# Performance work log

Hardware: AMD Instinct MI355X
Metric: run time of the kernel (lower is better)

Reference implementation:

```python
import jax, jax.numpy as jnp
import numpy as np

B, L, C = 2, 2048, 1024
DK, H = 64, 16

def setup_inputs() -> dict:
    key = jax.random.key(0)
    ks = jax.random.split(key, 12)
    def lin(kw, kb, out_dim, in_dim):
        w = jax.random.normal(kw, (out_dim, in_dim), jnp.float32) * (1.0 / np.sqrt(in_dim))
        b = jnp.zeros((out_dim,), jnp.float32)
        return w, b
    WQ_w, WQ_b = lin(ks[0], ks[1], DK * H, C)
    WK_w, WK_b = lin(ks[2], ks[3], DK * H, C)
    WV_w, WV_b = lin(ks[4], ks[5], DK * H, C)
    WO_w, WO_b = lin(ks[6], ks[7], C, DK * H)
    qx = jax.random.normal(ks[8], (B, L, C), jnp.float32)
    kx = jax.random.normal(ks[9], (B, L, C), jnp.float32)
    vx = jax.random.normal(ks[10], (B, L, C), jnp.float32)
    maskPAD = jax.random.randint(ks[11], (B, L, L), 0, 2, jnp.int32)
    return {"qx": qx, "kx": kx, "vx": vx, "maskPAD": maskPAD,
            "WQ_w": WQ_w, "WQ_b": WQ_b, "WK_w": WK_w, "WK_b": WK_b,
            "WV_w": WV_w, "WV_b": WV_b, "WO_w": WO_w, "WO_b": WO_b}

def reference(qx, kx, vx, maskPAD, WQ_w, WQ_b, WK_w, WK_b, WV_w, WV_b, WO_w, WO_b):
    Bq, qL, _ = qx.shape
    kvL = kx.shape[1]
    # projections -> [B, H, L, DK]
    q = (qx @ WQ_w.T + WQ_b).reshape(Bq, qL, H, DK).transpose(0, 2, 1, 3)
    k = (kx @ WK_w.T + WK_b).reshape(Bq, kvL, H, DK).transpose(0, 2, 1, 3)
    v = (vx @ WV_w.T + WV_b).reshape(Bq, kvL, H, DK).transpose(0, 2, 1, 3)
    scores = jnp.einsum('bhqd,bhkd->bhqk', q, k) / np.sqrt(DK).astype(np.float32)
    scores = jnp.where((maskPAD == 0)[:, None, :, :], jnp.float32(-2**15 + 1), scores)
    alpha = jax.nn.softmax(scores, axis=3)  # dropout p=0 (eval)
    z = jnp.einsum('bhqk,bhkd->bhqd', alpha, v)
    z = z.transpose(0, 2, 1, 3).reshape(Bq, qL, H * DK)
    return z @ WO_w.T + WO_b
```

## Files before the change

### kernel.cpp

```cpp
#include <hip/hip_runtime.h>
#include <stdint.h>
#include <math.h>

typedef short short8 __attribute__((ext_vector_type(8)));
typedef short short4v __attribute__((ext_vector_type(4)));
typedef float float4v __attribute__((ext_vector_type(4)));

static __device__ __forceinline__ float bf2f(uint16_t u) {
    union { uint32_t i; float f; } x; x.i = ((uint32_t)u) << 16; return x.f;
}
static __device__ __forceinline__ uint16_t f2bf(float f) {
    union { float f; uint32_t i; } x; x.f = f;
    uint32_t u = x.i;
    u += 0x7FFFu + ((u >> 16) & 1u);
    return (uint16_t)(u >> 16);
}
static __device__ __forceinline__ uint16_t f2bf_sane(float f) {
    uint16_t u = f2bf(f);
    if ((u & 0x7F80u) == 0x7F80u) u = 0;
    return u;
}
static __device__ __forceinline__ float san_f32(float f) {
    union { float f; uint32_t i; } x; x.f = f;
    if (((x.i >> 23) & 0xFFu) == 0xFFu) return 0.f;
    return x.f;
}
static __device__ __forceinline__ void gll16(const void* g, void* l) {
    __builtin_amdgcn_global_load_lds((const __attribute__((address_space(1))) void*)g,
                                     (__attribute__((address_space(3))) void*)l,
                                     16, 0, 0);
}
static __device__ __forceinline__ short8 load8(const void* p, size_t off, int fp32) {
    if (!fp32) return *(const short8*)((const uint16_t*)p + off);
    const float* f = (const float*)p + off;
    const float4v a = *(const float4v*)f;
    const float4v b = *(const float4v*)(f + 4);
    short8 r;
    r[0] = (short)f2bf(a[0]); r[1] = (short)f2bf(a[1]);
    r[2] = (short)f2bf(a[2]); r[3] = (short)f2bf(a[3]);
    r[4] = (short)f2bf(b[0]); r[5] = (short)f2bf(b[1]);
    r[6] = (short)f2bf(b[2]); r[7] = (short)f2bf(b[3]);
    return r;
}

static __device__ __forceinline__ float4v mfma16_bf16(short4v a, short4v b, float4v c) {
#if __has_builtin(__builtin_amdgcn_mfma_f32_16x16x16bf16_1k)
    return __builtin_amdgcn_mfma_f32_16x16x16bf16_1k(a, b, c, 0, 0, 0);
#else
    float4v d = c;
    asm volatile("v_mfma_f32_16x16x16_bf16 %0, %1, %2, %0"
                 : "+v"(d) : "v"(a), "v"(b));
    return d;
#endif
}

__global__ __launch_bounds__(256) void detect_kernel(const uint16_t* qx, int* flag)
{
    __shared__ int s;
    const int tid = threadIdx.x;
    if (tid == 0) s = 0;
    __syncthreads();
    int bad = 0;
#pragma unroll 8
    for (int i = 0; i < 64; ++i) {
        const uint16_t u = qx[tid * 64 + i];
        bad |= ((u & 0x7F80u) == 0x7F80u) ? 1 : 0;
    }
    if (bad) atomicOr(&s, 1);
    __syncthreads();
    if (tid == 0) *flag = s;
}

__global__ __launch_bounds__(256) void pack_kernel(
    const int* __restrict__ mask, uint64_t* __restrict__ mask64)
{
    const int wave = threadIdx.x >> 6, lane = threadIdx.x & 63;
    const int row = blockIdx.x * 4 + wave;
    const int* src = mask + (size_t)row * 2048;
#pragma unroll 4
    for (int j = 0; j < 32; ++j) {
        const int m = src[j * 64 + lane];
        const uint64_t bal = __ballot(m != 0);
        if (lane == 0) mask64[(size_t)row * 32 + j] = bal;
    }
}

__global__ __launch_bounds__(256) void convert_kernel(
    const void* qx, const void* kx, const void* vx,
    const void* wq, const void* wk, const void* wv, const void* wo,
    const void* bq, const void* bk, const void* bv, const void* bo,
    uint16_t* cIn, uint16_t* cW, uint16_t* cB, const int* flag)
{
    const int mode = *flag;
    if (!mode) return;
    const int z = blockIdx.z;
    if (z < 3) {
        const void* src = (z == 0) ? qx : (z == 1) ? kx : vx;
        uint16_t* dst = cIn + (size_t)z * 4194304;
#pragma unroll
        for (int it = 0; it < 8; ++it) {
            const int idx8 = (blockIdx.x * 8 + it) * 256 + threadIdx.x;
            *(short8*)(dst + (size_t)idx8 * 8) = load8(src, (size_t)idx8 * 8, 1);
        }
    } else if (z < 7) {
        const int t = z - 3;
        const void* src = (t == 0) ? wq : (t == 1) ? wk : (t == 2) ? wv : wo;
        uint16_t* dst = cW + (size_t)t * 1048576;
#pragma unroll
        for (int it = 0; it < 2; ++it) {
            const int idx8 = (blockIdx.x * 2 + it) * 256 + threadIdx.x;
            *(short8*)(dst + (size_t)idx8 * 8) = load8(src, (size_t)idx8 * 8, 1);
        }
    } else {
        const int idx8 = blockIdx.x * 256 + threadIdx.x;
        if (idx8 < 128) {
#pragma unroll
            for (int t = 0; t < 4; ++t) {
                const void* src = (t == 0) ? bq : (t == 1) ? bk : (t == 2) ? bv : bo;
                *(short8*)(cB + t * 1024 + idx8 * 8) = load8(src, (size_t)idx8 * 8, 1);
            }
        }
    }
}

template <int MI, int NI>
static __device__ __forceinline__ void gemm_tile(
    const uint16_t* __restrict__ A, const uint16_t* __restrict__ W,
    const uint16_t* __restrict__ bias, void* __restrict__ C,
    int c_fp32, float out_scale)
{
    constexpr int TM = MI * 32, TN = NI * 32;
    __shared__ __align__(16) uint16_t sA[TM * 32];
    __shared__ __align__(16) uint16_t sB[TN * 32];

    const int tid  = threadIdx.x;
    const int wave = tid >> 6;
    const int lane = tid & 63;
    const int quad = lane >> 4;
    const int l15  = lane & 15;
    const int m0 = blockIdx.y * TM;
    const int n0 = blockIdx.x * TN;
    const int wm = (wave >> 1) * (MI * 16);
    const int wn = (wave & 1) * (NI * 16);
    const int r16 = lane >> 2;
    const int ch  = lane & 3;

    float4v acc[MI][NI] = {};

    for (int k0 = 0; k0 < 1024; k0 += 32) {
        __syncthreads();
#pragma unroll
        for (int g = wave; g < TM / 16; g += 4)
            gll16(A + (size_t)(m0 + g * 16 + r16) * 1024 + k0 + ch * 8,
                  (char*)sA + (size_t)g * 1024);
#pragma unroll
        for (int g = wave; g < TN / 16; g += 4)
            gll16(W + (size_t)(n0 + g * 16 + r16) * 1024 + k0 + ch * 8,
                  (char*)sB + (size_t)g * 1024);
        asm volatile("s_waitcnt vmcnt(0)" ::: "memory");
        __syncthreads();

        short8 af[MI], bfr[NI];
#pragma unroll
        for (int i = 0; i < MI; ++i)
            af[i] = *(const short8*)&sA[(wm + i * 16 + l15) * 32 + quad * 8];
#pragma unroll
        for (int j = 0; j < NI; ++j)
            bfr[j] = *(const short8*)&sB[(wn + j * 16 + l15) * 32 + quad * 8];
#pragma unroll
        for (int mi = 0; mi < MI; ++mi)
#pragma unroll
            for (int ni = 0; ni < NI; ++ni)
                acc[mi][ni] = __builtin_amdgcn_mfma_f32_16x16x32_bf16(
                    af[mi], bfr[ni], acc[mi][ni], 0, 0, 0);
    }

#pragma unroll
    for (int ni = 0; ni < NI; ++ni) {
        const int n = n0 + wn + ni * 16 + l15;
        const float bv = bf2f(bias[n]);
#pragma unroll
        for (int mi = 0; mi < MI; ++mi) {
            const int mbase = m0 + wm + mi * 16 + quad * 4;
#pragma unroll
            for (int r = 0; r < 4; ++r) {
                const float v = (acc[mi][ni][r] + bv) * out_scale;
                const size_t idx = (size_t)(mbase + r) * 1024 + n;
                if (c_fp32) ((float*)C)[idx] = san_f32(v);
                else        ((uint16_t*)C)[idx] = f2bf_sane(v);
            }
        }
    }
}

__global__ __launch_bounds__(256) void qkv_kernel(
    const uint16_t* rqx, const uint16_t* rkx, const uint16_t* rvx,
    const uint16_t* rwq, const uint16_t* rwk, const uint16_t* rwv,
    const uint16_t* rbq, const uint16_t* rbk, const uint16_t* rbv,
    const uint16_t* cIn, const uint16_t* cW, const uint16_t* cB,
    uint16_t* Q, uint16_t* K, uint16_t* V, const int* flag)
{
    const int mode = *flag;
    const int z = blockIdx.z;
    const uint16_t* A = mode ? cIn + (size_t)z * 4194304
                             : ((z == 0) ? rqx : (z == 1) ? rkx : rvx);
    const uint16_t* W = mode ? cW + (size_t)z * 1048576
                             : ((z == 0) ? rwq : (z == 1) ? rwk : rwv);
    const uint16_t* b = mode ? cB + z * 1024
                             : ((z == 0) ? rbq : (z == 1) ? rbk : rbv);
    uint16_t* C = (z == 0) ? Q : (z == 1) ? K : V;
    const float sc = (z == 0) ? 0.125f : 1.0f;
    gemm_tile<4, 4>(A, W, b, C, 0, sc);
}

__global__ __launch_bounds__(256) void out_kernel(
    const uint16_t* Z, const uint16_t* rwo, const uint16_t* rbo,
    const uint16_t* cW, const uint16_t* cB, void* out, const int* flag)
{
    const int mode = *flag;
    const uint16_t* W = mode ? cW + 3 * 1048576 : rwo;
    const uint16_t* b = mode ? cB + 3 * 1024 : rbo;
    gemm_tile<2, 4>(Z, W, b, out, mode, 1.0f);
}

__global__ __launch_bounds__(256) void vtrans_kernel(
    const uint16_t* __restrict__ Vp, uint16_t* __restrict__ Vt)
{
    __shared__ __align__(16) uint16_t t[64][72];
    const int tid = threadIdx.x;
    const int lt = blockIdx.x, h = blockIdx.y, b = blockIdx.z;
#pragma unroll
    for (int p = 0; p < 2; ++p) {
        const int r = p * 32 + (tid >> 3);
        const int c = (tid & 7) * 8;
        *(short8*)&t[r][c] =
            *(const short8*)(Vp + (size_t)(b * 2048 + lt * 64 + r) * 1024 + h * 64 + c);
    }
    __syncthreads();
#pragma unroll
    for (int p = 0; p < 2; ++p) {
        const int d = p * 32 + (tid >> 3);
        const int c = (tid & 7) * 8;
        short8 v;
#pragma unroll
        for (int j = 0; j < 8; ++j) v[j] = (short)t[c + j][d];
        *(short8*)(Vt + (size_t)((b * 16 + h) * 64 + d) * 2048 + lt * 64 + c) = v;
    }
}

#define VS 72

__global__ __launch_bounds__(256, 4) void attn_kernel(
    const uint16_t* __restrict__ Q, const uint16_t* __restrict__ Kp,
    const uint16_t* __restrict__ Vt, const uint64_t* __restrict__ mask64,
    uint16_t* __restrict__ Oa, uint16_t* __restrict__ Ob,
    float* __restrict__ lpart)
{
    __shared__ __align__(16) uint16_t sK[64 * VS];
    __shared__ __align__(16) uint16_t sV[64 * VS];

    const int tid = threadIdx.x;
    const int wave = tid >> 6, lane = tid & 63;
    const int quad = lane >> 4, l15 = lane & 15;
    const int qt = blockIdx.x, h = blockIdx.y;
    const int b = blockIdx.z & 1, half = blockIdx.z >> 1;
    const int q0 = qt * 128;
    const int qw = q0 + wave * 32;

    const int srow = tid >> 2;
    const int sc0  = tid & 3;

    short8 qf[2][2];
#pragma unroll
    for (int mi = 0; mi < 2; ++mi)
#pragma unroll
        for (int kk = 0; kk < 2; ++kk)
            qf[mi][kk] = *(const short8*)(Q + (size_t)(b * 2048 + qw + mi * 16 + l15) * 1024
                                            + h * 64 + (quad + 4 * kk) * 8);

    const uint64_t* mrow[2];
#pragma unroll
    for (int mj = 0; mj < 2; ++mj)
        mrow[mj] = mask64 + (size_t)(b * 2048 + qw + mj * 16 + l15) * 32;

    float4v oaccT[4][2] = {};
    float lsum[2] = {};

    const int kt_lo = half * 16, kt_hi = kt_lo + 16;
    for (int kt = kt_lo; kt < kt_hi; ++kt) {
        const int k0 = kt * 64;
        const short8 kx0 = *(const short8*)(Kp + (size_t)(b * 2048 + k0 + srow) * 1024 + h * 64 + sc0 * 8);
        const short8 kx1 = *(const short8*)(Kp + (size_t)(b * 2048 + k0 + srow) * 1024 + h * 64 + (sc0 + 4) * 8);
        const short8 vx0 = *(const short8*)(Vt + (size_t)((b * 16 + h) * 64 + srow) * 2048 + k0 + sc0 * 8);
        const short8 vx1 = *(const short8*)(Vt + (size_t)((b * 16 + h) * 64 + srow) * 2048 + k0 + (sc0 + 4) * 8);
        const uint64_t mw0 = mrow[0][kt];
        const uint64_t mw1 = mrow[1][kt];
        __syncthreads();
        *(short8*)&sK[srow * VS + sc0 * 8]       = kx0;
        *(short8*)&sK[srow * VS + (sc0 + 4) * 8] = kx1;
        *(short8*)&sV[srow * VS + sc0 * 8]       = vx0;
        *(short8*)&sV[srow * VS + (sc0 + 4) * 8] = vx1;
        __syncthreads();

        float4v sacc[2][4] = {};
#pragma unroll
        for (int ni = 0; ni < 4; ++ni) {
            const int row = ni * 16 + l15;
#pragma unroll
            for (int kk = 0; kk < 2; ++kk) {
                const short8 kf = *(const short8*)&sK[row * VS + (quad + 4 * kk) * 8];
                sacc[0][ni] = __builtin_amdgcn_mfma_f32_16x16x32_bf16(kf, qf[0][kk], sacc[0][ni], 0, 0, 0);
                sacc[1][ni] = __builtin_amdgcn_mfma_f32_16x16x32_bf16(kf, qf[1][kk], sacc[1][ni], 0, 0, 0);
            }
        }

        short4v pf[2][4];
#pragma unroll
        for (int mj = 0; mj < 2; ++mj) {
            const uint64_t mw = mj ? mw1 : mw0;
#pragma unroll
            for (int ni = 0; ni < 4; ++ni) {
                const uint32_t nib = (uint32_t)(mw >> (ni * 16 + quad * 4)) & 0xFu;
                short4v t;
#pragma unroll
                for (int r = 0; r < 4; ++r) {
                    const float p = (nib >> r) & 1u ? __expf(sacc[mj][ni][r]) : 0.f;
                    lsum[mj] += p;
                    t[r] = (short)f2bf(p);
                }
                pf[mj][ni] = t;
            }
        }

#pragma unroll
        for (int di = 0; di < 4; ++di) {
            const int row = di * 16 + l15;
#pragma unroll
            for (int ni = 0; ni < 4; ++ni) {
                const short4v vf = *(const short4v*)&sV[row * VS + ni * 16 + quad * 4];
                oaccT[di][0] = mfma16_bf16(vf, pf[0][ni], oaccT[di][0]);
                oaccT[di][1] = mfma16_bf16(vf, pf[1][ni], oaccT[di][1]);
            }
        }
    }

#if !__has_builtin(__builtin_amdgcn_mfma_f32_16x16x16bf16_1k)
    asm volatile("s_nop 7\ns_nop 7\ns_nop 7" ::: "memory");
#endif

#pragma unroll
    for (int mj = 0; mj < 2; ++mj) {
        lsum[mj] += __shfl_xor(lsum[mj], 16);
        lsum[mj] += __shfl_xor(lsum[mj], 32);
    }

    uint16_t* Op = half ? Ob : Oa;
#pragma unroll
    for (int mj = 0; mj < 2; ++mj) {
        const int qrow = qw + mj * 16 + l15;
#pragma unroll
        for (int di = 0; di < 4; ++di) {
            short4v o;
#pragma unroll
            for (int r = 0; r < 4; ++r) o[r] = (short)f2bf(oaccT[di][mj][r]);
            *(short4v*)(Op + (size_t)(b * 2048 + qrow) * 1024 + h * 64 + di * 16 + quad * 4) = o;
        }
        if (quad == 0)
            lpart[half * 65536 + (b * 16 + h) * 2048 + qrow] = lsum[mj];
    }
}

__global__ __launch_bounds__(256) void combine_kernel(
    const uint16_t* __restrict__ Oa, const uint16_t* __restrict__ Ob,
    const float* __restrict__ lpart, uint16_t* __restrict__ Z)
{
    const int e8 = blockIdx.x * 256 + threadIdx.x;
    const int flat = e8 * 8;
    const int bh_row = flat >> 10;
    const int h = (flat >> 6) & 15;
    const int b = bh_row >> 11;
    const int row = bh_row & 2047;
    const int lidx = (b * 16 + h) * 2048 + row;
    const float inv = 1.0f / fmaxf(lpart[lidx] + lpart[65536 + lidx], 1e-37f);
    const short8 a = *(const short8*)(Oa + flat);
    const short8 c = *(const short8*)(Ob + flat);
    short8 o;
#pragma unroll
    for (int j = 0; j < 8; ++j)
        o[j] = (short)f2bf_sane((bf2f((uint16_t)a[j]) + bf2f((uint16_t)c[j])) * inv);
    *(short8*)(Z + flat) = o;
}

extern "C" void kernel_launch(void* const* d_in, const int* in_sizes, int n_in,
                              void* d_out, int out_size, void* d_ws, size_t ws_size,
                              hipStream_t stream)
{
    const void* qx  = d_in[0];
    const void* kx  = d_in[1];
    const void* vx  = d_in[2];
    const int*  msk = (const int*)d_in[3];

    char* ws = (char*)d_ws;
    const size_t MB = 1024 * 1024;
    uint16_t* cIn = (uint16_t*)(ws);
    uint16_t* cW  = (uint16_t*)(ws + 24 * MB);
    uint16_t* cB  = (uint16_t*)(ws + 32 * MB);
    int*      flg = (int*)(ws + 32 * MB + 16 * 1024);
    uint16_t* Qb  = (uint16_t*)(ws + 33 * MB);
    uint16_t* Kb  = (uint16_t*)(ws + 41 * MB);
    uint16_t* Vb  = (uint16_t*)(ws + 49 * MB);
    uint64_t* m64 = (uint64_t*)(ws + 57 * MB);
    uint16_t* Vt  = (uint16_t*)(ws + 8 * MB);
    uint16_t* Oa  = (uint16_t*)(ws);
    uint16_t* Ob  = (uint16_t*)(ws + 16 * MB);
    float*    lp  = (float*)(ws + 49 * MB);
    uint16_t* Zb  = Oa;

    detect_kernel<<<1, 256, 0, stream>>>((const uint16_t*)qx, flg);
    pack_kernel<<<1024, 256, 0, stream>>>(msk, m64);
    convert_kernel<<<dim3(256, 1, 8), 256, 0, stream>>>(
        qx, kx, vx, d_in[4], d_in[6], d_in[8], d_in[10],
        d_in[5], d_in[7], d_in[9], d_in[11], cIn, cW, cB, flg);
    qkv_kernel<<<dim3(8, 32, 3), 256, 0, stream>>>(
        (const uint16_t*)qx, (const uint16_t*)kx, (const uint16_t*)vx,
        (const uint16_t*)d_in[4], (const uint16_t*)d_in[6], (const uint16_t*)d_in[8],
        (const uint16_t*)d_in[5], (const uint16_t*)d_in[7], (const uint16_t*)d_in[9],
        cIn, cW, cB, Qb, Kb, Vb, flg);
    vtrans_kernel<<<dim3(32, 16, 2), 256, 0, stream>>>(Vb, Vt);
    attn_kernel<<<dim3(16, 16, 4), 256, 0, stream>>>(Qb, Kb, Vt, m64, Oa, Ob, lp);
    combine_kernel<<<4096, 256, 0, stream>>>(Oa, Ob, lp, Zb);
    out_kernel<<<dim3(8, 64), 256, 0, stream>>>(
        Zb, (const uint16_t*)d_in[10], (const uint16_t*)d_in[11], cW, cB, d_out, flg);
}
```

Baseline: 305.5 us.

## Fuse mask packing into QKV launch and streamline softmax exponent and row sums

```diff
diff --git a/kernel.cpp b/kernel.cpp
--- a/kernel.cpp
+++ b/kernel.cpp
@@ -5,6 +5,7 @@
 typedef short short8 __attribute__((ext_vector_type(8)));
 typedef short short4v __attribute__((ext_vector_type(4)));
 typedef float float4v __attribute__((ext_vector_type(4)));
+typedef unsigned int uint2v __attribute__((ext_vector_type(2)));
 
 static __device__ __forceinline__ float bf2f(uint16_t u) {
     union { uint32_t i; float f; } x; x.i = ((uint32_t)u) << 16; return x.f;
@@ -42,7 +43,17 @@
     r[6] = (short)f2bf(b[2]); r[7] = (short)f2bf(b[3]);
     return r;
 }
-
+static __device__ __forceinline__ float fast_exp2(float x) {
+#if __has_builtin(__builtin_amdgcn_exp2f)
+    return __builtin_amdgcn_exp2f(x);
+#else
+    return exp2f(x);
+#endif
+}
+static __device__ __forceinline__ uint32_t pkbf(float a, float b) {
+    union { float f; uint32_t u; } xa, xb; xa.f = a; xb.f = b;
+    return __builtin_amdgcn_perm(xb.u + 0x8000u, xa.u + 0x8000u, 0x07060302u);
+}
 static __device__ __forceinline__ float4v mfma16_bf16(short4v a, short4v b, float4v c) {
 #if __has_builtin(__builtin_amdgcn_mfma_f32_16x16x16bf16_1k)
     return __builtin_amdgcn_mfma_f32_16x16x16bf16_1k(a, b, c, 0, 0, 0);
@@ -69,20 +80,6 @@
     if (bad) atomicOr(&s, 1);
     __syncthreads();
     if (tid == 0) *flag = s;
-}
-
-__global__ __launch_bounds__(256) void pack_kernel(
-    const int* __restrict__ mask, uint64_t* __restrict__ mask64)
-{
-    const int wave = threadIdx.x >> 6, lane = threadIdx.x & 63;
-    const int row = blockIdx.x * 4 + wave;
-    const int* src = mask + (size_t)row * 2048;
-#pragma unroll 4
-    for (int j = 0; j < 32; ++j) {
-        const int m = src[j * 64 + lane];
-        const uint64_t bal = __ballot(m != 0);
-        if (lane == 0) mask64[(size_t)row * 32 + j] = bal;
-    }
 }
 
 __global__ __launch_bounds__(256) void convert_kernel(
@@ -193,15 +190,33 @@
     }
 }
 
+#define QSCALE 0.180336880f
+
 __global__ __launch_bounds__(256) void qkv_kernel(
     const uint16_t* rqx, const uint16_t* rkx, const uint16_t* rvx,
     const uint16_t* rwq, const uint16_t* rwk, const uint16_t* rwv,
     const uint16_t* rbq, const uint16_t* rbk, const uint16_t* rbv,
     const uint16_t* cIn, const uint16_t* cW, const uint16_t* cB,
-    uint16_t* Q, uint16_t* K, uint16_t* V, const int* flag)
-{
+    uint16_t* Q, uint16_t* K, uint16_t* V, const int* flag,
+    const int* __restrict__ mask, uint64_t* __restrict__ mask64)
+{
+    const int z = blockIdx.z;
+    if (z == 3) {
+        const int wave = threadIdx.x >> 6, lane = threadIdx.x & 63;
+        const int bid = blockIdx.y * 8 + blockIdx.x;
+#pragma unroll
+        for (int rr = 0; rr < 4; ++rr) {
+            const int row = bid * 16 + wave * 4 + rr;
+            const int* src = mask + (size_t)row * 2048;
+#pragma unroll 4
+            for (int j = 0; j < 32; ++j) {
+                const uint64_t bal = __ballot(src[j * 64 + lane] != 0);
+                if (lane == 0) mask64[(size_t)row * 32 + j] = bal;
+            }
+        }
+        return;
+    }
     const int mode = *flag;
-    const int z = blockIdx.z;
     const uint16_t* A = mode ? cIn + (size_t)z * 4194304
                              : ((z == 0) ? rqx : (z == 1) ? rkx : rvx);
     const uint16_t* W = mode ? cW + (size_t)z * 1048576
@@ -209,7 +224,7 @@
     const uint16_t* b = mode ? cB + z * 1024
                              : ((z == 0) ? rbq : (z == 1) ? rbk : rbv);
     uint16_t* C = (z == 0) ? Q : (z == 1) ? K : V;
-    const float sc = (z == 0) ? 0.125f : 1.0f;
+    const float sc = (z == 0) ? QSCALE : 1.0f;
     gemm_tile<4, 4>(A, W, b, C, 0, sc);
 }
 
@@ -283,8 +298,12 @@
     for (int mj = 0; mj < 2; ++mj)
         mrow[mj] = mask64 + (size_t)(b * 2048 + qw + mj * 16 + l15) * 32;
 
+    short4v ones4;
+#pragma unroll
+    for (int j = 0; j < 4; ++j) ones4[j] = (short)0x3F80;
+
     float4v oaccT[4][2] = {};
-    float lsum[2] = {};
+    float4v lacc[2] = {};
 
     const int kt_lo = half * 16, kt_hi = kt_lo + 16;
     for (int kt = kt_lo; kt < kt_hi; ++kt) {
@@ -321,14 +340,14 @@
 #pragma unroll
             for (int ni = 0; ni < 4; ++ni) {
                 const uint32_t nib = (uint32_t)(mw >> (ni * 16 + quad * 4)) & 0xFu;
-                short4v t;
-#pragma unroll
-                for (int r = 0; r < 4; ++r) {
-                    const float p = (nib >> r) & 1u ? __expf(sacc[mj][ni][r]) : 0.f;
-                    lsum[mj] += p;
-                    t[r] = (short)f2bf(p);
-                }
-                pf[mj][ni] = t;
+                float p[4];
+#pragma unroll
+                for (int r = 0; r < 4; ++r)
+                    p[r] = (nib >> r) & 1u ? fast_exp2(sacc[mj][ni][r]) : 0.f;
+                union { uint2v u; short4v s; } cv;
+                cv.u[0] = pkbf(p[0], p[1]);
+                cv.u[1] = pkbf(p[2], p[3]);
+                pf[mj][ni] = cv.s;
             }
         }
 
@@ -342,18 +361,17 @@
                 oaccT[di][1] = mfma16_bf16(vf, pf[1][ni], oaccT[di][1]);
             }
         }
+#pragma unroll
+        for (int mj = 0; mj < 2; ++mj)
+#pragma unroll
+            for (int ni = 0; ni < 4; ++ni)
+                lacc[mj] = mfma16_bf16(ones4, pf[mj][ni], lacc[mj]);
     }
 
 #if !__has_builtin(__builtin_amdgcn_mfma_f32_16x16x16bf16_1k)
     asm volatile("s_nop 7\ns_nop 7\ns_nop 7" ::: "memory");
 #endif
 
-#pragma unroll
-    for (int mj = 0; mj < 2; ++mj) {
-        lsum[mj] += __shfl_xor(lsum[mj], 16);
-        lsum[mj] += __shfl_xor(lsum[mj], 32);
-    }
-
     uint16_t* Op = half ? Ob : Oa;
 #pragma unroll
     for (int mj = 0; mj < 2; ++mj) {
@@ -366,7 +384,7 @@
             *(short4v*)(Op + (size_t)(b * 2048 + qrow) * 1024 + h * 64 + di * 16 + quad * 4) = o;
         }
         if (quad == 0)
-            lpart[half * 65536 + (b * 16 + h) * 2048 + qrow] = lsum[mj];
+            lpart[half * 65536 + (b * 16 + h) * 2048 + qrow] = lacc[mj][0];
     }
 }
 
@@ -417,15 +435,14 @@
     uint16_t* Zb  = Oa;
 
     detect_kernel<<<1, 256, 0, stream>>>((const uint16_t*)qx, flg);
-    pack_kernel<<<1024, 256, 0, stream>>>(msk, m64);
     convert_kernel<<<dim3(256, 1, 8), 256, 0, stream>>>(
         qx, kx, vx, d_in[4], d_in[6], d_in[8], d_in[10],
         d_in[5], d_in[7], d_in[9], d_in[11], cIn, cW, cB, flg);
-    qkv_kernel<<<dim3(8, 32, 3), 256, 0, stream>>>(
+    qkv_kernel<<<dim3(8, 32, 4), 256, 0, stream>>>(
         (const uint16_t*)qx, (const uint16_t*)kx, (const uint16_t*)vx,
         (const uint16_t*)d_in[4], (const uint16_t*)d_in[6], (const uint16_t*)d_in[8],
         (const uint16_t*)d_in[5], (const uint16_t*)d_in[7], (const uint16_t*)d_in[9],
-        cIn, cW, cB, Qb, Kb, Vb, flg);
+        cIn, cW, cB, Qb, Kb, Vb, flg, msk, m64);
     vtrans_kernel<<<dim3(32, 16, 2), 256, 0, stream>>>(Vb, Vt);
     attn_kernel<<<dim3(16, 16, 4), 256, 0, stream>>>(Qb, Kb, Vt, m64, Oa, Ob, lp);
     combine_kernel<<<4096, 256, 0, stream>>>(Oa, Ob, lp, Zb);
```

New measurement: 334.7 us. 9.6% more time.
